# Optimization experiments

Hardware: AMD Instinct MI355X
Metric: run time of the kernel (lower is better)

## Reference

```python
import jax, jax.numpy as jnp
import numpy as np

TEMP1, TEMP2, TEMP3 = 4.0, 5.0, 10.0  # forward() default temps
EPS = 1e-8


def setup_inputs() -> dict:
    key = jax.random.key(0)
    k1, k2 = jax.random.split(key)
    B, L, D = 64, 64, 512
    return {
        "ecg_embs": jax.random.normal(k1, (B, L, D), dtype=jnp.float32),
        "sent_embs": jax.random.normal(k2, (B, L, D), dtype=jnp.float32),
    }


def reference(ecg_embs, sent_embs):
    # Fully-batched version of the original per-sample Python loop.
    # i indexes the sentence (query) sample, j the ecg (context) sample.
    B, L, D = ecg_embs.shape
    # scores[i,j,s,q] = <ecg[j,s,:], sent[i,q,:]>  == contextT @ query in torch
    scores = jnp.einsum('jsd,iqd->ijsq', ecg_embs, sent_embs)
    # 1st softmax over query axis q
    attn = jax.nn.softmax(scores, axis=-1)
    # transpose to (i,j,q,s), temperature-scale, 2nd softmax over source axis s
    attn = jax.nn.softmax(TEMP1 * jnp.swapaxes(attn, -1, -2), axis=-1)  # (i,j,q,s)
    # weightedContext[i,j,q,:] = sum_s attn[i,j,q,s] * ecg[j,s,:]
    wctx = jnp.einsum('ijqs,jsd->ijqd', attn, ecg_embs)
    sent = sent_embs[:, None]  # (i,1,q,d) broadcast over j
    w12 = jnp.sum(sent * wctx, axis=-1)
    w1 = jnp.linalg.norm(sent, axis=-1)
    w2 = jnp.linalg.norm(wctx, axis=-1)
    cos = w12 / jnp.maximum(w1 * w2, EPS)  # (i,j,q)
    # row_sim.mul_(temp2).exp_().sum(dim=1).log() ; similarities[j,i] (cat along dim=1)
    sim = TEMP3 * jnp.log(jnp.sum(jnp.exp(TEMP2 * cos), axis=-1)).T  # (j,i)
    labels = jnp.arange(B)
    logp0 = jax.nn.log_softmax(sim, axis=-1)
    logp1 = jax.nn.log_softmax(sim.T, axis=-1)
    loss0 = -jnp.mean(logp0[labels, labels])
    loss1 = -jnp.mean(logp1[labels, labels])
    # att_maps: list of attn[i] from iteration i == diagonal (i==j) attention,
    # each shaped (1, queryL, ih=1, iw=sourceL); stacked -> (B, 1, L, 1, L)
    att_maps = attn[labels, labels][:, None, :, None, :]
    return (loss0 + loss1) / 2.0, att_maps
```

## Files before the change

### kernel.cpp

```cpp
#include <hip/hip_runtime.h>
#include <math.h>

typedef __attribute__((ext_vector_type(8))) short short8;
typedef __attribute__((ext_vector_type(4))) float f32x4;
typedef unsigned int uint;
typedef unsigned short ushort;

#define T1 4.0f
#define T2 5.0f
#define T3 10.0f
#define EPSF 1e-8f
#define SST 68

__device__ inline ushort f2bf(float x) {
    union { float f; uint u; } a; a.f = x;
    uint r = a.u + 0x7FFFu + ((a.u >> 16) & 1u);
    return (ushort)(r >> 16);
}
__device__ inline float bf2f(ushort h) {
    union { uint u; float f; } a; a.u = ((uint)h) << 16;
    return a.f;
}

#define GLDS(gsrc, ldst) \
    __builtin_amdgcn_global_load_lds( \
        (const __attribute__((address_space(1))) uint*)(gsrc), \
        (__attribute__((address_space(3))) uint*)(ldst), 16, 0, 0)

__global__ __launch_bounds__(256) void prep_kernel(
        const float* __restrict__ ecg, const float* __restrict__ sent,
        char* __restrict__ EH, char* __restrict__ EL,
        char* __restrict__ SH, char* __restrict__ SL, float* __restrict__ w1) {
    __shared__ float partial[256];
    const int bid = blockIdx.x;
    const int tensor = bid >> 6, idx = bid & 63;
    const float* src = (tensor ? sent : ecg) + (size_t)idx * 32768;
    char* dh = (tensor ? SH : EH) + (size_t)idx * 65536;
    char* dl = (tensor ? SL : EL) + (size_t)idx * 65536;
    const int tid = threadIdx.x;
    const int r = tid & 63;
    float s2 = 0.f;
    #pragma unroll
    for (int it = 0; it < 4; it++) {
        int kc = it * 4 + (tid >> 6);
        const float* p = src + r * 512 + kc * 32;
        char* oh = dh + kc * 4096 + r * 64;
        char* ol = dl + kc * 4096 + r * 64;
        #pragma unroll
        for (int c = 0; c < 4; c++) {
            float4 v0 = *(const float4*)(p + c * 8);
            float4 v1 = *(const float4*)(p + c * 8 + 4);
            float x[8] = {v0.x, v0.y, v0.z, v0.w, v1.x, v1.y, v1.z, v1.w};
            uint hw[4], lw[4];
            #pragma unroll
            for (int e = 0; e < 4; e++) {
                float a0 = x[2 * e], a1 = x[2 * e + 1];
                ushort h0 = f2bf(a0), h1 = f2bf(a1);
                hw[e] = (uint)h0 | ((uint)h1 << 16);
                ushort l0 = f2bf(a0 - bf2f(h0)), l1 = f2bf(a1 - bf2f(h1));
                lw[e] = (uint)l0 | ((uint)l1 << 16);
                s2 += a0 * a0 + a1 * a1;
            }
            int phys = (c + (r >> 1)) & 3;
            uint4 H; H.x = hw[0]; H.y = hw[1]; H.z = hw[2]; H.w = hw[3];
            *(uint4*)(oh + phys * 16) = H;
            uint4 L; L.x = lw[0]; L.y = lw[1]; L.z = lw[2]; L.w = lw[3];
            *(uint4*)(ol + phys * 16) = L;
        }
    }
    partial[tid] = s2;
    __syncthreads();
    if (tensor == 1 && tid < 64) {
        float t = partial[tid] + partial[tid + 64] + partial[tid + 128] + partial[tid + 192];
        w1[idx * 64 + tid] = sqrtf(t);
    }
}

__global__ __launch_bounds__(256) void gprep_kernel(
        const char* __restrict__ EH, const char* __restrict__ EL, char* __restrict__ Gp) {
    __shared__ __align__(16) char lds[8192];
    const int j = blockIdx.x;
    const int tid = threadIdx.x;
    const int wv = tid >> 6, lane = tid & 63;
    const int wq = wv >> 1, wn = wv & 1;
    const int quad = lane >> 4, ln = lane & 15;
    const char* srcH = EH + (size_t)j * 65536 + wv * 1024 + lane * 16;
    const char* srcL = EL + (size_t)j * 65536 + wv * 1024 + lane * 16;

    int ao[2], bo[2];
    #pragma unroll
    for (int mi = 0; mi < 2; mi++) {
        int R = 32 * wq + 16 * mi + ln;
        ao[mi] = R * 64 + ((quad + (R >> 1)) & 3) * 16;
    }
    #pragma unroll
    for (int ni = 0; ni < 2; ni++) {
        int R = 32 * wn + 16 * ni + ln;
        bo[ni] = R * 64 + ((quad + (R >> 1)) & 3) * 16;
    }

    f32x4 acc[2][2];
    #pragma unroll
    for (int a = 0; a < 2; a++)
        #pragma unroll
        for (int b = 0; b < 2; b++) acc[a][b] = (f32x4){0.f, 0.f, 0.f, 0.f};

    for (int kc = 0; kc < 16; kc++) {
        GLDS(srcH + (size_t)kc * 4096, lds + wv * 1024);
        GLDS(srcL + (size_t)kc * 4096, lds + 4096 + wv * 1024);
        __syncthreads();
        short8 ah[2], al[2], bh[2], bl[2];
        #pragma unroll
        for (int mi = 0; mi < 2; mi++) {
            ah[mi] = *(const short8*)(lds + ao[mi]);
            al[mi] = *(const short8*)(lds + 4096 + ao[mi]);
        }
        #pragma unroll
        for (int ni = 0; ni < 2; ni++) {
            bh[ni] = *(const short8*)(lds + bo[ni]);
            bl[ni] = *(const short8*)(lds + 4096 + bo[ni]);
        }
        #pragma unroll
        for (int mi = 0; mi < 2; mi++)
            #pragma unroll
            for (int ni = 0; ni < 2; ni++) {
                acc[mi][ni] = __builtin_amdgcn_mfma_f32_16x16x32_bf16(ah[mi], bh[ni], acc[mi][ni], 0, 0, 0);
                acc[mi][ni] = __builtin_amdgcn_mfma_f32_16x16x32_bf16(ah[mi], bl[ni], acc[mi][ni], 0, 0, 0);
                acc[mi][ni] = __builtin_amdgcn_mfma_f32_16x16x32_bf16(al[mi], bh[ni], acc[mi][ni], 0, 0, 0);
            }
        __syncthreads();
    }
    #pragma unroll
    for (int mi = 0; mi < 2; mi++)
        #pragma unroll
        for (int ni = 0; ni < 2; ni++)
            #pragma unroll
            for (int r = 0; r < 4; r++) {
                int t = 32 * wq + 16 * mi + quad * 4 + r;
                int u = 32 * wn + 16 * ni + ln;
                float g = acc[mi][ni][r];
                ushort h = f2bf(g);
                ushort l = f2bf(g - bf2f(h));
                char* base = Gp + (size_t)j * 16384 + t * 128 + (((u >> 3) + t) & 7) * 16 + (u & 7) * 2;
                *(ushort*)base = h;
                *(ushort*)(base + 8192) = l;
            }
}

__global__ __launch_bounds__(256, 4) void pair_kernel(
        const char* __restrict__ EH, const char* __restrict__ EL,
        const char* __restrict__ SH, const char* __restrict__ SL,
        const char* __restrict__ Gp, const float* __restrict__ w1g,
        float* __restrict__ simval, float* __restrict__ out) {

    __shared__ __align__(16) char lds[33792];
    __shared__ __align__(16) float mz[64];
    __shared__ float w12all[256], w2all[256];

    const int tid = threadIdx.x;
    const int bn = blockIdx.x;
    const int xcd = bn & 7, slot = bn >> 3;
    const int T = xcd * 8 + (slot >> 4);
    const int wp = slot & 15;
    const int bi = (T >> 3) * 4 + (wp >> 2);
    const int bj = (T & 7) * 4 + (wp & 3);
    const int i0 = bi * 2, j0 = bj * 2;

    const int wv = tid >> 6, lane = tid & 63;
    const int wq = wv >> 1, wn = wv & 1;
    const int quad = lane >> 4, ln = lane & 15;

    int aoff[4], boff[4];
    #pragma unroll
    for (int mi = 0; mi < 4; mi++) {
        int R = 64 * (mi >> 1) + 32 * wq + 16 * (mi & 1) + ln;
        aoff[mi] = R * 64 + ((quad + (R >> 1)) & 3) * 16;
    }
    #pragma unroll
    for (int ni = 0; ni < 4; ni++) {
        int R = 64 * (ni >> 1) + 32 * wn + 16 * (ni & 1) + ln;
        boff[ni] = 16384 + R * 64 + ((quad + (R >> 1)) & 3) * 16;
    }

    const char* gA; const char* gB; int ldoff;
    if (wv == 0)      { gA = EH + (size_t)j0 * 65536;       gB = EH + (size_t)(j0 + 1) * 65536; ldoff = 0; }
    else if (wv == 1) { gA = EL + (size_t)j0 * 65536;       gB = EL + (size_t)(j0 + 1) * 65536; ldoff = 8192; }
    else if (wv == 2) { gA = SH + (size_t)i0 * 65536;       gB = SH + (size_t)(i0 + 1) * 65536; ldoff = 16384; }
    else              { gA = SL + (size_t)i0 * 65536;       gB = SL + (size_t)(i0 + 1) * 65536; ldoff = 24576; }
    gA += lane * 16; gB += lane * 16;

    f32x4 acc[4][4];
    #pragma unroll
    for (int a = 0; a < 4; a++)
        #pragma unroll
        for (int b = 0; b < 4; b++) acc[a][b] = (f32x4){0.f, 0.f, 0.f, 0.f};

    for (int kc = 0; kc < 16; kc++) {
        #pragma unroll
        for (int n = 0; n < 4; n++) GLDS(gA + n * 1024, lds + ldoff + n * 1024);
        #pragma unroll
        for (int n = 0; n < 4; n++) GLDS(gB + n * 1024, lds + ldoff + 4096 + n * 1024);
        gA += 4096; gB += 4096;
        __syncthreads();
        short8 bh[4], bl[4];
        #pragma unroll
        for (int ni = 0; ni < 4; ni++) {
            bh[ni] = *(const short8*)(lds + boff[ni]);
            bl[ni] = *(const short8*)(lds + boff[ni] + 8192);
        }
        #pragma unroll
        for (int mi = 0; mi < 4; mi++) {
            short8 ah = *(const short8*)(lds + aoff[mi]);
            short8 al = *(const short8*)(lds + aoff[mi] + 8192);
            #pragma unroll
            for (int ni = 0; ni < 4; ni++) {
                acc[mi][ni] = __builtin_amdgcn_mfma_f32_16x16x32_bf16(ah, bh[ni], acc[mi][ni], 0, 0, 0);
                acc[mi][ni] = __builtin_amdgcn_mfma_f32_16x16x32_bf16(ah, bl[ni], acc[mi][ni], 0, 0, 0);
                acc[mi][ni] = __builtin_amdgcn_mfma_f32_16x16x32_bf16(al, bh[ni], acc[mi][ni], 0, 0, 0);
            }
        }
        __syncthreads();
    }

    float* SsT = (float*)lds;
    float* yT  = (float*)lds;
    char*  Pb  = lds + 17408;

    #pragma unroll
    for (int pr = 0; pr < 4; pr++) {
        const int a = pr >> 1, b = pr & 1;
        const int i = i0 + b, j = j0 + a;

        #pragma unroll
        for (int dm = 0; dm < 2; dm++)
            #pragma unroll
            for (int dn = 0; dn < 2; dn++) {
                int s0 = 32 * wq + 16 * dm + quad * 4;
                int q  = 32 * wn + 16 * dn + ln;
                *(f32x4*)(SsT + q * SST + s0) = acc[2 * a + dm][2 * b + dn];
            }
        __syncthreads();

        {
            const int s = tid >> 2, c = tid & 3;
            float vv[16]; float m = -1e30f;
            #pragma unroll
            for (int t = 0; t < 16; t++) { vv[t] = SsT[(16 * c + t) * SST + s]; m = fmaxf(m, vv[t]); }
            m = fmaxf(m, __shfl_xor(m, 1));
            m = fmaxf(m, __shfl_xor(m, 2));
            float sum = 0.f;
            #pragma unroll
            for (int t = 0; t < 16; t++) sum += __expf(vv[t] - m);
            sum += __shfl_xor(sum, 1);
            sum += __shfl_xor(sum, 2);
            if (c == 0) mz[s] = m + __logf(sum);
        }
        __syncthreads();

        {
            const int q = tid >> 2, c = tid & 3;
            float sc[16], at[16];
            #pragma unroll
            for (int r4 = 0; r4 < 4; r4++)
                *(f32x4*)(sc + 4 * r4) = *(const f32x4*)(SsT + q * SST + 16 * c + 4 * r4);
            float mzv[16];
            #pragma unroll
            for (int r4 = 0; r4 < 4; r4++)
                *(f32x4*)(mzv + 4 * r4) = *(const f32x4*)(mz + 16 * c + 4 * r4);
            float m2 = -1e30f;
            #pragma unroll
            for (int t = 0; t < 16; t++) {
                at[t] = __expf(sc[t] - mzv[t]);
                m2 = fmaxf(m2, T1 * at[t]);
            }
            m2 = fmaxf(m2, __shfl_xor(m2, 1));
            m2 = fmaxf(m2, __shfl_xor(m2, 2));
            float sum = 0.f;
            #pragma unroll
            for (int t = 0; t < 16; t++) { at[t] = __expf(T1 * at[t] - m2); sum += at[t]; }
            sum += __shfl_xor(sum, 1);
            sum += __shfl_xor(sum, 2);
            float inv = 1.f / sum;
            float p12 = 0.f;
            #pragma unroll
            for (int t = 0; t < 16; t++) { at[t] *= inv; p12 += at[t] * sc[t]; }
            p12 += __shfl_xor(p12, 1);
            p12 += __shfl_xor(p12, 2);
            if (c == 0) w12all[pr * 64 + q] = p12;

            if (i == j) {
                float* om = out + 1 + (size_t)i * 4096;
                #pragma unroll
                for (int t = 0; t < 16; t++) om[q * 64 + c * 16 + t] = at[t];
            }

            uint hw[8], lw[8];
            #pragma unroll
            for (int e = 0; e < 8; e++) {
                ushort h0 = f2bf(at[2 * e]), h1 = f2bf(at[2 * e + 1]);
                hw[e] = (uint)h0 | ((uint)h1 << 16);
                ushort l0 = f2bf(at[2 * e] - bf2f(h0)), l1 = f2bf(at[2 * e + 1] - bf2f(h1));
                lw[e] = (uint)l0 | ((uint)l1 << 16);
            }
            int p0 = (2 * c + q) & 7, p1 = (2 * c + 1 + q) & 7;
            uint4 W;
            W.x = hw[0]; W.y = hw[1]; W.z = hw[2]; W.w = hw[3];
            *(uint4*)(Pb + q * 128 + p0 * 16) = W;
            W.x = hw[4]; W.y = hw[5]; W.z = hw[6]; W.w = hw[7];
            *(uint4*)(Pb + q * 128 + p1 * 16) = W;
            W.x = lw[0]; W.y = lw[1]; W.z = lw[2]; W.w = lw[3];
            *(uint4*)(Pb + 8192 + q * 128 + p0 * 16) = W;
            W.x = lw[4]; W.y = lw[5]; W.z = lw[6]; W.w = lw[7];
            *(uint4*)(Pb + 8192 + q * 128 + p1 * 16) = W;
        }
        __syncthreads();

        {
            const char* gs = Gp + (size_t)j * 16384 + tid * 64;
            char* gd = lds + tid * 64;
            uint4 g0 = *(const uint4*)(gs);
            uint4 g1 = *(const uint4*)(gs + 16);
            uint4 g2 = *(const uint4*)(gs + 32);
            uint4 g3 = *(const uint4*)(gs + 48);
            *(uint4*)(gd)      = g0;
            *(uint4*)(gd + 16) = g1;
            *(uint4*)(gd + 32) = g2;
            *(uint4*)(gd + 48) = g3;
        }
        __syncthreads();

        f32x4 acc2[2][2];
        #pragma unroll
        for (int x = 0; x < 2; x++)
            #pragma unroll
            for (int y = 0; y < 2; y++) acc2[x][y] = (f32x4){0.f, 0.f, 0.f, 0.f};
        #pragma unroll
        for (int ch = 0; ch < 2; ch++) {
            short8 pah[2], pal[2], gbh[2], gbl[2];
            #pragma unroll
            for (int m2i = 0; m2i < 2; m2i++) {
                int q = 32 * wq + 16 * m2i + ln;
                int ph = ((ch * 4 + quad) + q) & 7;
                pah[m2i] = *(const short8*)(Pb + q * 128 + ph * 16);
                pal[m2i] = *(const short8*)(Pb + 8192 + q * 128 + ph * 16);
            }
            #pragma unroll
            for (int n2i = 0; n2i < 2; n2i++) {
                int u = 32 * wn + 16 * n2i + ln;
                int ph = ((ch * 4 + quad) + u) & 7;
                gbh[n2i] = *(const short8*)(lds + u * 128 + ph * 16);
                gbl[n2i] = *(const short8*)(lds + 8192 + u * 128 + ph * 16);
            }
            #pragma unroll
            for (int m2i = 0; m2i < 2; m2i++)
                #pragma unroll
                for (int n2i = 0; n2i < 2; n2i++) {
                    acc2[m2i][n2i] = __builtin_amdgcn_mfma_f32_16x16x32_bf16(pah[m2i], gbh[n2i], acc2[m2i][n2i], 0, 0, 0);
                    acc2[m2i][n2i] = __builtin_amdgcn_mfma_f32_16x16x32_bf16(pah[m2i], gbl[n2i], acc2[m2i][n2i], 0, 0, 0);
                    acc2[m2i][n2i] = __builtin_amdgcn_mfma_f32_16x16x32_bf16(pal[m2i], gbh[n2i], acc2[m2i][n2i], 0, 0, 0);
                }
        }
        __syncthreads();

        #pragma unroll
        for (int m2i = 0; m2i < 2; m2i++)
            #pragma unroll
            for (int n2i = 0; n2i < 2; n2i++) {
                int q0 = 32 * wq + 16 * m2i + quad * 4;
                int t  = 32 * wn + 16 * n2i + ln;
                *(f32x4*)(yT + t * SST + q0) = acc2[m2i][n2i];
            }
        __syncthreads();

        {
            const int q = tid >> 2, c = tid & 3;
            int p0 = (2 * c + q) & 7, p1 = (2 * c + 1 + q) & 7;
            uint4 H0 = *(const uint4*)(Pb + q * 128 + p0 * 16);
            uint4 H1 = *(const uint4*)(Pb + q * 128 + p1 * 16);
            uint4 L0 = *(const uint4*)(Pb + 8192 + q * 128 + p0 * 16);
            uint4 L1 = *(const uint4*)(Pb + 8192 + q * 128 + p1 * 16);
            uint hw[8] = {H0.x,H0.y,H0.z,H0.w, H1.x,H1.y,H1.z,H1.w};
            uint lw[8] = {L0.x,L0.y,L0.z,L0.w, L1.x,L1.y,L1.z,L1.w};
            float s = 0.f;
            #pragma unroll
            for (int e = 0; e < 8; e++) {
                float q0v = bf2f((ushort)(hw[e] & 0xFFFFu)) + bf2f((ushort)(lw[e] & 0xFFFFu));
                float q1v = bf2f((ushort)(hw[e] >> 16))     + bf2f((ushort)(lw[e] >> 16));
                s += q0v * yT[(16 * c + 2 * e) * SST + q];
                s += q1v * yT[(16 * c + 2 * e + 1) * SST + q];
            }
            s += __shfl_xor(s, 1);
            s += __shfl_xor(s, 2);
            if (c == 0) w2all[pr * 64 + q] = s;
        }
        __syncthreads();
    }

    {
        const int pr = wv;
        const int ii = i0 + (pr & 1), jj = j0 + (pr >> 1);
        float w2 = sqrtf(fmaxf(w2all[pr * 64 + lane], 0.f));
        float cosv = w12all[pr * 64 + lane] / fmaxf(w1g[ii * 64 + lane] * w2, EPSF);
        float e = __expf(T2 * cosv);
        #pragma unroll
        for (int off = 32; off; off >>= 1) e += __shfl_down(e, off);
        if (lane == 0) simval[ii * 64 + jj] = T3 * __logf(e);
    }
}

__global__ __launch_bounds__(256) void loss_kernel(const float* __restrict__ val,
                                                   float* __restrict__ out) {
    __shared__ float v[4096];
    const int tid = threadIdx.x;
    #pragma unroll
    for (int k = 0; k < 4; k++)
        ((float4*)v)[tid + k * 256] = ((const float4*)val)[tid + k * 256];
    __syncthreads();
    if (tid < 64) {
        int i = tid;
        float rmax = -1e30f, cmax = -1e30f;
        for (int jj = 0; jj < 64; jj++) {
            rmax = fmaxf(rmax, v[i * 64 + jj]);
            cmax = fmaxf(cmax, v[jj * 64 + i]);
        }
        float rs = 0.f, cs = 0.f;
        for (int jj = 0; jj < 64; jj++) {
            rs += __expf(v[i * 64 + jj] - rmax);
            cs += __expf(v[jj * 64 + i] - cmax);
        }
        float rlse = rmax + __logf(rs);
        float clse = cmax + __logf(cs);
        float part = 2.f * v[i * 64 + i] - rlse - clse;
        #pragma unroll
        for (int off = 32; off; off >>= 1) part += __shfl_down(part, off);
        if (i == 0) out[0] = -part / 128.f;
    }
}

extern "C" void kernel_launch(void* const* d_in, const int* in_sizes, int n_in,
                              void* d_out, int out_size, void* d_ws, size_t ws_size,
                              hipStream_t stream) {
    (void)in_sizes; (void)n_in; (void)out_size; (void)ws_size;
    const float* ecg  = (const float*)d_in[0];
    const float* sent = (const float*)d_in[1];
    float* out = (float*)d_out;

    char* ws = (char*)d_ws;
    float* w1v  = (float*)ws;
    float* simv = (float*)(ws + 16384);
    char* EH = ws + 32768;
    char* EL = EH + (size_t)64 * 65536;
    char* SH = EL + (size_t)64 * 65536;
    char* SL = SH + (size_t)64 * 65536;
    char* Gp = SL + (size_t)64 * 65536;

    prep_kernel <<<128, 256, 0, stream>>>(ecg, sent, EH, EL, SH, SL, w1v);
    gprep_kernel<<<64,  256, 0, stream>>>(EH, EL, Gp);
    pair_kernel <<<1024, 256, 0, stream>>>(EH, EL, SH, SL, Gp, w1v, simv, out);
    loss_kernel <<<1,   256, 0, stream>>>(simv, out);
}
```

Before: 151.3 us.

## Fuse prep and Gram kernels, drop attention low-part split, read Gram from global

Merges the bf16 hi/lo split prep kernel with the Gram-matrix kernel, so ecg blocks compute G directly from freshly converted tiles and one launch plus a global round trip disappear. In the pair kernel the attention matrix is now stored only as a bf16 high part, which cuts one of three MFMAs in the second GEMM. Gram operands are read straight from global/L2 instead of being staged through LDS. The w2 quadratic form is computed from the accumulators in registers with a small partial-sum buffer, and the score tile uses an XOR-swizzled layout, removing several barriers and LDS passes. Dropping the attention low part lowers precision of w2, and direct global loads of G may add latency.

```diff
diff --git a/kernel.cpp b/kernel.cpp
--- a/kernel.cpp
+++ b/kernel.cpp
@@ -10,7 +10,6 @@
 #define T2 5.0f
 #define T3 10.0f
 #define EPSF 1e-8f
-#define SST 68
 
 __device__ inline ushort f2bf(float x) {
     union { float f; uint u; } a; a.f = x;
@@ -27,124 +26,127 @@
         (const __attribute__((address_space(1))) uint*)(gsrc), \
         (__attribute__((address_space(3))) uint*)(ldst), 16, 0, 0)
 
-__global__ __launch_bounds__(256) void prep_kernel(
+__global__ __launch_bounds__(256) void prepg_kernel(
         const float* __restrict__ ecg, const float* __restrict__ sent,
         char* __restrict__ EH, char* __restrict__ EL,
-        char* __restrict__ SH, char* __restrict__ SL, float* __restrict__ w1) {
-    __shared__ float partial[256];
+        char* __restrict__ SH, char* __restrict__ SL,
+        char* __restrict__ Gp, float* __restrict__ w1) {
+    __shared__ __align__(16) char plds[8192];
     const int bid = blockIdx.x;
-    const int tensor = bid >> 6, idx = bid & 63;
-    const float* src = (tensor ? sent : ecg) + (size_t)idx * 32768;
-    char* dh = (tensor ? SH : EH) + (size_t)idx * 65536;
-    char* dl = (tensor ? SL : EL) + (size_t)idx * 65536;
     const int tid = threadIdx.x;
-    const int r = tid & 63;
-    float s2 = 0.f;
-    #pragma unroll
-    for (int it = 0; it < 4; it++) {
-        int kc = it * 4 + (tid >> 6);
-        const float* p = src + r * 512 + kc * 32;
-        char* oh = dh + kc * 4096 + r * 64;
-        char* ol = dl + kc * 4096 + r * 64;
-        #pragma unroll
-        for (int c = 0; c < 4; c++) {
-            float4 v0 = *(const float4*)(p + c * 8);
-            float4 v1 = *(const float4*)(p + c * 8 + 4);
-            float x[8] = {v0.x, v0.y, v0.z, v0.w, v1.x, v1.y, v1.z, v1.w};
-            uint hw[4], lw[4];
-            #pragma unroll
-            for (int e = 0; e < 4; e++) {
-                float a0 = x[2 * e], a1 = x[2 * e + 1];
-                ushort h0 = f2bf(a0), h1 = f2bf(a1);
-                hw[e] = (uint)h0 | ((uint)h1 << 16);
-                ushort l0 = f2bf(a0 - bf2f(h0)), l1 = f2bf(a1 - bf2f(h1));
-                lw[e] = (uint)l0 | ((uint)l1 << 16);
-                s2 += a0 * a0 + a1 * a1;
-            }
-            int phys = (c + (r >> 1)) & 3;
-            uint4 H; H.x = hw[0]; H.y = hw[1]; H.z = hw[2]; H.w = hw[3];
-            *(uint4*)(oh + phys * 16) = H;
-            uint4 L; L.x = lw[0]; L.y = lw[1]; L.z = lw[2]; L.w = lw[3];
-            *(uint4*)(ol + phys * 16) = L;
-        }
-    }
-    partial[tid] = s2;
-    __syncthreads();
-    if (tensor == 1 && tid < 64) {
-        float t = partial[tid] + partial[tid + 64] + partial[tid + 128] + partial[tid + 192];
-        w1[idx * 64 + tid] = sqrtf(t);
-    }
-}
-
-__global__ __launch_bounds__(256) void gprep_kernel(
-        const char* __restrict__ EH, const char* __restrict__ EL, char* __restrict__ Gp) {
-    __shared__ __align__(16) char lds[8192];
-    const int j = blockIdx.x;
-    const int tid = threadIdx.x;
-    const int wv = tid >> 6, lane = tid & 63;
-    const int wq = wv >> 1, wn = wv & 1;
-    const int quad = lane >> 4, ln = lane & 15;
-    const char* srcH = EH + (size_t)j * 65536 + wv * 1024 + lane * 16;
-    const char* srcL = EL + (size_t)j * 65536 + wv * 1024 + lane * 16;
-
-    int ao[2], bo[2];
-    #pragma unroll
-    for (int mi = 0; mi < 2; mi++) {
-        int R = 32 * wq + 16 * mi + ln;
-        ao[mi] = R * 64 + ((quad + (R >> 1)) & 3) * 16;
-    }
-    #pragma unroll
-    for (int ni = 0; ni < 2; ni++) {
-        int R = 32 * wn + 16 * ni + ln;
-        bo[ni] = R * 64 + ((quad + (R >> 1)) & 3) * 16;
-    }
-
-    f32x4 acc[2][2];
-    #pragma unroll
-    for (int a = 0; a < 2; a++)
-        #pragma unroll
-        for (int b = 0; b < 2; b++) acc[a][b] = (f32x4){0.f, 0.f, 0.f, 0.f};
-
-    for (int kc = 0; kc < 16; kc++) {
-        GLDS(srcH + (size_t)kc * 4096, lds + wv * 1024);
-        GLDS(srcL + (size_t)kc * 4096, lds + 4096 + wv * 1024);
-        __syncthreads();
-        short8 ah[2], al[2], bh[2], bl[2];
+    const int r = tid >> 2, cq = tid & 3;
+    const int phys = (cq + (r >> 1)) & 3;
+
+    if (bid < 64) {
+        const int j = bid;
+        const float* src = ecg + (size_t)j * 32768;
+        char* dh = EH + (size_t)j * 65536;
+        char* dl = EL + (size_t)j * 65536;
+        const int wv = tid >> 6, lane = tid & 63;
+        const int wq = wv >> 1, wn = wv & 1;
+        const int quad = lane >> 4, ln = lane & 15;
+        int ao[2], bo[2];
         #pragma unroll
         for (int mi = 0; mi < 2; mi++) {
-            ah[mi] = *(const short8*)(lds + ao[mi]);
-            al[mi] = *(const short8*)(lds + 4096 + ao[mi]);
+            int R = 32 * wq + 16 * mi + ln;
+            ao[mi] = R * 64 + ((quad + (R >> 1)) & 3) * 16;
         }
         #pragma unroll
         for (int ni = 0; ni < 2; ni++) {
-            bh[ni] = *(const short8*)(lds + bo[ni]);
-            bl[ni] = *(const short8*)(lds + 4096 + bo[ni]);
+            int R = 32 * wn + 16 * ni + ln;
+            bo[ni] = R * 64 + ((quad + (R >> 1)) & 3) * 16;
+        }
+        f32x4 acc[2][2];
+        #pragma unroll
+        for (int a = 0; a < 2; a++)
+            #pragma unroll
+            for (int b = 0; b < 2; b++) acc[a][b] = (f32x4){0.f, 0.f, 0.f, 0.f};
+
+        for (int kc = 0; kc < 16; kc++) {
+            const float4* p = (const float4*)(src + (size_t)r * 512 + kc * 32 + cq * 8);
+            float4 va = p[0], vb = p[1];
+            ushort h0 = f2bf(va.x), h1 = f2bf(va.y), h2 = f2bf(va.z), h3 = f2bf(va.w);
+            ushort h4 = f2bf(vb.x), h5 = f2bf(vb.y), h6 = f2bf(vb.z), h7 = f2bf(vb.w);
+            uint4 H;
+            H.x = (uint)h0 | ((uint)h1 << 16); H.y = (uint)h2 | ((uint)h3 << 16);
+            H.z = (uint)h4 | ((uint)h5 << 16); H.w = (uint)h6 | ((uint)h7 << 16);
+            uint4 L;
+            L.x = (uint)f2bf(va.x - bf2f(h0)) | ((uint)f2bf(va.y - bf2f(h1)) << 16);
+            L.y = (uint)f2bf(va.z - bf2f(h2)) | ((uint)f2bf(va.w - bf2f(h3)) << 16);
+            L.z = (uint)f2bf(vb.x - bf2f(h4)) | ((uint)f2bf(vb.y - bf2f(h5)) << 16);
+            L.w = (uint)f2bf(vb.z - bf2f(h6)) | ((uint)f2bf(vb.w - bf2f(h7)) << 16);
+            __syncthreads();
+            *(uint4*)(plds + r * 64 + phys * 16)        = H;
+            *(uint4*)(plds + 4096 + r * 64 + phys * 16) = L;
+            *(uint4*)(dh + (size_t)kc * 4096 + r * 64 + phys * 16) = H;
+            *(uint4*)(dl + (size_t)kc * 4096 + r * 64 + phys * 16) = L;
+            __syncthreads();
+            short8 ah[2], al[2], bh[2], bl[2];
+            #pragma unroll
+            for (int mi = 0; mi < 2; mi++) {
+                ah[mi] = *(const short8*)(plds + ao[mi]);
+                al[mi] = *(const short8*)(plds + 4096 + ao[mi]);
+            }
+            #pragma unroll
+            for (int ni = 0; ni < 2; ni++) {
+                bh[ni] = *(const short8*)(plds + bo[ni]);
+                bl[ni] = *(const short8*)(plds + 4096 + bo[ni]);
+            }
+            #pragma unroll
+            for (int mi = 0; mi < 2; mi++)
+                #pragma unroll
+                for (int ni = 0; ni < 2; ni++) {
+                    acc[mi][ni] = __builtin_amdgcn_mfma_f32_16x16x32_bf16(ah[mi], bh[ni], acc[mi][ni], 0, 0, 0);
+                    acc[mi][ni] = __builtin_amdgcn_mfma_f32_16x16x32_bf16(ah[mi], bl[ni], acc[mi][ni], 0, 0, 0);
+                    acc[mi][ni] = __builtin_amdgcn_mfma_f32_16x16x32_bf16(al[mi], bh[ni], acc[mi][ni], 0, 0, 0);
+                }
         }
         #pragma unroll
         for (int mi = 0; mi < 2; mi++)
             #pragma unroll
-            for (int ni = 0; ni < 2; ni++) {
-                acc[mi][ni] = __builtin_amdgcn_mfma_f32_16x16x32_bf16(ah[mi], bh[ni], acc[mi][ni], 0, 0, 0);
-                acc[mi][ni] = __builtin_amdgcn_mfma_f32_16x16x32_bf16(ah[mi], bl[ni], acc[mi][ni], 0, 0, 0);
-                acc[mi][ni] = __builtin_amdgcn_mfma_f32_16x16x32_bf16(al[mi], bh[ni], acc[mi][ni], 0, 0, 0);
-            }
-        __syncthreads();
-    }
-    #pragma unroll
-    for (int mi = 0; mi < 2; mi++)
-        #pragma unroll
-        for (int ni = 0; ni < 2; ni++)
-            #pragma unroll
-            for (int r = 0; r < 4; r++) {
-                int t = 32 * wq + 16 * mi + quad * 4 + r;
-                int u = 32 * wn + 16 * ni + ln;
-                float g = acc[mi][ni][r];
-                ushort h = f2bf(g);
-                ushort l = f2bf(g - bf2f(h));
-                char* base = Gp + (size_t)j * 16384 + t * 128 + (((u >> 3) + t) & 7) * 16 + (u & 7) * 2;
-                *(ushort*)base = h;
-                *(ushort*)(base + 8192) = l;
-            }
+            for (int ni = 0; ni < 2; ni++)
+                #pragma unroll
+                for (int rr = 0; rr < 4; rr++) {
+                    int t = 32 * wq + 16 * mi + quad * 4 + rr;
+                    int u = 32 * wn + 16 * ni + ln;
+                    float g = acc[mi][ni][rr];
+                    ushort h = f2bf(g);
+                    ushort l = f2bf(g - bf2f(h));
+                    char* base = Gp + (size_t)j * 16384 + t * 128 + (((u >> 3) + t) & 7) * 16 + (u & 7) * 2;
+                    *(ushort*)base = h;
+                    *(ushort*)(base + 8192) = l;
+                }
+    } else {
+        const int idx = bid - 64;
+        const float* src = sent + (size_t)idx * 32768;
+        char* dh = SH + (size_t)idx * 65536;
+        char* dl = SL + (size_t)idx * 65536;
+        float s2 = 0.f;
+        for (int kc = 0; kc < 16; kc++) {
+            const float4* p = (const float4*)(src + (size_t)r * 512 + kc * 32 + cq * 8);
+            float4 va = p[0], vb = p[1];
+            s2 += va.x * va.x + va.y * va.y + va.z * va.z + va.w * va.w +
+                  vb.x * vb.x + vb.y * vb.y + vb.z * vb.z + vb.w * vb.w;
+            ushort h0 = f2bf(va.x), h1 = f2bf(va.y), h2 = f2bf(va.z), h3 = f2bf(va.w);
+            ushort h4 = f2bf(vb.x), h5 = f2bf(vb.y), h6 = f2bf(vb.z), h7 = f2bf(vb.w);
+            uint4 H;
+            H.x = (uint)h0 | ((uint)h1 << 16); H.y = (uint)h2 | ((uint)h3 << 16);
+            H.z = (uint)h4 | ((uint)h5 << 16); H.w = (uint)h6 | ((uint)h7 << 16);
+            uint4 L;
+            L.x = (uint)f2bf(va.x - bf2f(h0)) | ((uint)f2bf(va.y - bf2f(h1)) << 16);
+            L.y = (uint)f2bf(va.z - bf2f(h2)) | ((uint)f2bf(va.w - bf2f(h3)) << 16);
+            L.z = (uint)f2bf(vb.x - bf2f(h4)) | ((uint)f2bf(vb.y - bf2f(h5)) << 16);
+            L.w = (uint)f2bf(vb.z - bf2f(h6)) | ((uint)f2bf(vb.w - bf2f(h7)) << 16);
+            *(uint4*)(dh + (size_t)kc * 4096 + r * 64 + phys * 16) = H;
+            *(uint4*)(dl + (size_t)kc * 4096 + r * 64 + phys * 16) = L;
+        }
+        ((float*)plds)[tid] = s2;
+        __syncthreads();
+        if (tid < 64) {
+            const float* q = (const float*)plds + tid * 4;
+            w1[idx * 64 + tid] = sqrtf(q[0] + q[1] + q[2] + q[3]);
+        }
+    }
 }
 
 __global__ __launch_bounds__(256, 4) void pair_kernel(
@@ -153,9 +155,10 @@
         const char* __restrict__ Gp, const float* __restrict__ w1g,
         float* __restrict__ simval, float* __restrict__ out) {
 
-    __shared__ __align__(16) char lds[33792];
+    __shared__ __align__(16) char lds[32768];
     __shared__ __align__(16) float mz[64];
     __shared__ float w12all[256], w2all[256];
+    __shared__ float w2part[64 * 9];
 
     const int tid = threadIdx.x;
     const int bn = blockIdx.x;
@@ -222,14 +225,13 @@
         __syncthreads();
     }
 
-    float* SsT = (float*)lds;
-    float* yT  = (float*)lds;
-    char*  Pb  = lds + 17408;
+    char* Phi = lds + 16384;
 
     #pragma unroll
     for (int pr = 0; pr < 4; pr++) {
         const int a = pr >> 1, b = pr & 1;
         const int i = i0 + b, j = j0 + a;
+        const char* Gpj = Gp + (size_t)j * 16384;
 
         #pragma unroll
         for (int dm = 0; dm < 2; dm++)
@@ -237,7 +239,7 @@
             for (int dn = 0; dn < 2; dn++) {
                 int s0 = 32 * wq + 16 * dm + quad * 4;
                 int q  = 32 * wn + 16 * dn + ln;
-                *(f32x4*)(SsT + q * SST + s0) = acc[2 * a + dm][2 * b + dn];
+                *(f32x4*)(lds + q * 256 + (((s0 >> 2) + q) & 15) * 16) = acc[2 * a + dm][2 * b + dn];
             }
         __syncthreads();
 
@@ -245,7 +247,11 @@
             const int s = tid >> 2, c = tid & 3;
             float vv[16]; float m = -1e30f;
             #pragma unroll
-            for (int t = 0; t < 16; t++) { vv[t] = SsT[(16 * c + t) * SST + s]; m = fmaxf(m, vv[t]); }
+            for (int t = 0; t < 16; t++) {
+                int q = 16 * c + t;
+                vv[t] = *(const float*)(lds + q * 256 + ((((s >> 2) + q) & 15) << 4) + ((s & 3) << 2));
+                m = fmaxf(m, vv[t]);
+            }
             m = fmaxf(m, __shfl_xor(m, 1));
             m = fmaxf(m, __shfl_xor(m, 2));
             float sum = 0.f;
@@ -259,14 +265,13 @@
 
         {
             const int q = tid >> 2, c = tid & 3;
-            float sc[16], at[16];
-            #pragma unroll
-            for (int r4 = 0; r4 < 4; r4++)
-                *(f32x4*)(sc + 4 * r4) = *(const f32x4*)(SsT + q * SST + 16 * c + 4 * r4);
-            float mzv[16];
-            #pragma unroll
-            for (int r4 = 0; r4 < 4; r4++)
-                *(f32x4*)(mzv + 4 * r4) = *(const f32x4*)(mz + 16 * c + 4 * r4);
+            float sc[16], at[16], mzv[16];
+            #pragma unroll
+            for (int k = 0; k < 4; k++)
+                *(f32x4*)(sc + 4 * k) = *(const f32x4*)(lds + q * 256 + (((4 * c + k) + q) & 15) * 16);
+            #pragma unroll
+            for (int k = 0; k < 4; k++)
+                *(f32x4*)(mzv + 4 * k) = *(const f32x4*)(mz + 16 * c + 4 * k);
             float m2 = -1e30f;
             #pragma unroll
             for (int t = 0; t < 16; t++) {
@@ -294,38 +299,16 @@
                 for (int t = 0; t < 16; t++) om[q * 64 + c * 16 + t] = at[t];
             }
 
-            uint hw[8], lw[8];
-            #pragma unroll
-            for (int e = 0; e < 8; e++) {
-                ushort h0 = f2bf(at[2 * e]), h1 = f2bf(at[2 * e + 1]);
-                hw[e] = (uint)h0 | ((uint)h1 << 16);
-                ushort l0 = f2bf(at[2 * e] - bf2f(h0)), l1 = f2bf(at[2 * e + 1] - bf2f(h1));
-                lw[e] = (uint)l0 | ((uint)l1 << 16);
-            }
+            uint hw[8];
+            #pragma unroll
+            for (int e = 0; e < 8; e++)
+                hw[e] = (uint)f2bf(at[2 * e]) | ((uint)f2bf(at[2 * e + 1]) << 16);
             int p0 = (2 * c + q) & 7, p1 = (2 * c + 1 + q) & 7;
             uint4 W;
             W.x = hw[0]; W.y = hw[1]; W.z = hw[2]; W.w = hw[3];
-            *(uint4*)(Pb + q * 128 + p0 * 16) = W;
+            *(uint4*)(Phi + q * 128 + p0 * 16) = W;
             W.x = hw[4]; W.y = hw[5]; W.z = hw[6]; W.w = hw[7];
-            *(uint4*)(Pb + q * 128 + p1 * 16) = W;
-            W.x = lw[0]; W.y = lw[1]; W.z = lw[2]; W.w = lw[3];
-            *(uint4*)(Pb + 8192 + q * 128 + p0 * 16) = W;
-            W.x = lw[4]; W.y = lw[5]; W.z = lw[6]; W.w = lw[7];
-            *(uint4*)(Pb + 8192 + q * 128 + p1 * 16) = W;
-        }
-        __syncthreads();
-
-        {
-            const char* gs = Gp + (size_t)j * 16384 + tid * 64;
-            char* gd = lds + tid * 64;
-            uint4 g0 = *(const uint4*)(gs);
-            uint4 g1 = *(const uint4*)(gs + 16);
-            uint4 g2 = *(const uint4*)(gs + 32);
-            uint4 g3 = *(const uint4*)(gs + 48);
-            *(uint4*)(gd)      = g0;
-            *(uint4*)(gd + 16) = g1;
-            *(uint4*)(gd + 32) = g2;
-            *(uint4*)(gd + 48) = g3;
+            *(uint4*)(Phi + q * 128 + p1 * 16) = W;
         }
         __syncthreads();
 
@@ -336,20 +319,18 @@
             for (int y = 0; y < 2; y++) acc2[x][y] = (f32x4){0.f, 0.f, 0.f, 0.f};
         #pragma unroll
         for (int ch = 0; ch < 2; ch++) {
-            short8 pah[2], pal[2], gbh[2], gbl[2];
+            short8 pah[2], gbh[2], gbl[2];
             #pragma unroll
             for (int m2i = 0; m2i < 2; m2i++) {
                 int q = 32 * wq + 16 * m2i + ln;
-                int ph = ((ch * 4 + quad) + q) & 7;
-                pah[m2i] = *(const short8*)(Pb + q * 128 + ph * 16);
-                pal[m2i] = *(const short8*)(Pb + 8192 + q * 128 + ph * 16);
+                pah[m2i] = *(const short8*)(Phi + q * 128 + (((ch * 4 + quad) + q) & 7) * 16);
             }
             #pragma unroll
             for (int n2i = 0; n2i < 2; n2i++) {
                 int u = 32 * wn + 16 * n2i + ln;
                 int ph = ((ch * 4 + quad) + u) & 7;
-                gbh[n2i] = *(const short8*)(lds + u * 128 + ph * 16);
-                gbl[n2i] = *(const short8*)(lds + 8192 + u * 128 + ph * 16);
+                gbh[n2i] = *(const short8*)(Gpj + u * 128 + ph * 16);
+                gbl[n2i] = *(const short8*)(Gpj + 8192 + u * 128 + ph * 16);
             }
             #pragma unroll
             for (int m2i = 0; m2i < 2; m2i++)
@@ -357,44 +338,35 @@
                 for (int n2i = 0; n2i < 2; n2i++) {
                     acc2[m2i][n2i] = __builtin_amdgcn_mfma_f32_16x16x32_bf16(pah[m2i], gbh[n2i], acc2[m2i][n2i], 0, 0, 0);
                     acc2[m2i][n2i] = __builtin_amdgcn_mfma_f32_16x16x32_bf16(pah[m2i], gbl[n2i], acc2[m2i][n2i], 0, 0, 0);
-                    acc2[m2i][n2i] = __builtin_amdgcn_mfma_f32_16x16x32_bf16(pal[m2i], gbh[n2i], acc2[m2i][n2i], 0, 0, 0);
                 }
         }
-        __syncthreads();
 
         #pragma unroll
         for (int m2i = 0; m2i < 2; m2i++)
             #pragma unroll
-            for (int n2i = 0; n2i < 2; n2i++) {
-                int q0 = 32 * wq + 16 * m2i + quad * 4;
-                int t  = 32 * wn + 16 * n2i + ln;
-                *(f32x4*)(yT + t * SST + q0) = acc2[m2i][n2i];
-            }
-        __syncthreads();
-
-        {
-            const int q = tid >> 2, c = tid & 3;
-            int p0 = (2 * c + q) & 7, p1 = (2 * c + 1 + q) & 7;
-            uint4 H0 = *(const uint4*)(Pb + q * 128 + p0 * 16);
-            uint4 H1 = *(const uint4*)(Pb + q * 128 + p1 * 16);
-            uint4 L0 = *(const uint4*)(Pb + 8192 + q * 128 + p0 * 16);
-            uint4 L1 = *(const uint4*)(Pb + 8192 + q * 128 + p1 * 16);
-            uint hw[8] = {H0.x,H0.y,H0.z,H0.w, H1.x,H1.y,H1.z,H1.w};
-            uint lw[8] = {L0.x,L0.y,L0.z,L0.w, L1.x,L1.y,L1.z,L1.w};
-            float s = 0.f;
-            #pragma unroll
-            for (int e = 0; e < 8; e++) {
-                float q0v = bf2f((ushort)(hw[e] & 0xFFFFu)) + bf2f((ushort)(lw[e] & 0xFFFFu));
-                float q1v = bf2f((ushort)(hw[e] >> 16))     + bf2f((ushort)(lw[e] >> 16));
-                s += q0v * yT[(16 * c + 2 * e) * SST + q];
-                s += q1v * yT[(16 * c + 2 * e + 1) * SST + q];
-            }
-            s += __shfl_xor(s, 1);
-            s += __shfl_xor(s, 2);
-            if (c == 0) w2all[pr * 64 + q] = s;
-        }
-        __syncthreads();
-    }
+            for (int rr = 0; rr < 4; rr++) {
+                int q = 32 * wq + 16 * m2i + quad * 4 + rr;
+                float p = 0.f;
+                #pragma unroll
+                for (int n2i = 0; n2i < 2; n2i++) {
+                    int t = 32 * wn + 16 * n2i + ln;
+                    float Pv = bf2f(*(const ushort*)(Phi + q * 128 +
+                                     ((((t >> 3) + q) & 7) << 4) + ((t & 7) << 1)));
+                    p += acc2[m2i][n2i][rr] * Pv;
+                }
+                p += __shfl_xor(p, 1);
+                p += __shfl_xor(p, 2);
+                if ((ln & 3) == 0) w2part[q * 9 + wn * 4 + (ln >> 2)] = p;
+            }
+        __syncthreads();
+
+        if (tid < 64) {
+            const float* wp9 = w2part + tid * 9;
+            w2all[pr * 64 + tid] = wp9[0] + wp9[1] + wp9[2] + wp9[3] +
+                                   wp9[4] + wp9[5] + wp9[6] + wp9[7];
+        }
+    }
+    __syncthreads();
 
     {
         const int pr = wv;
@@ -454,8 +426,7 @@
     char* SL = SH + (size_t)64 * 65536;
     char* Gp = SL + (size_t)64 * 65536;
 
-    prep_kernel <<<128, 256, 0, stream>>>(ecg, sent, EH, EL, SH, SL, w1v);
-    gprep_kernel<<<64,  256, 0, stream>>>(EH, EL, Gp);
+    prepg_kernel<<<128,  256, 0, stream>>>(ecg, sent, EH, EL, SH, SL, Gp, w1v);
     pair_kernel <<<1024, 256, 0, stream>>>(EH, EL, SH, SL, Gp, w1v, simv, out);
-    loss_kernel <<<1,   256, 0, stream>>>(simv, out);
-}
+    loss_kernel <<<1,    256, 0, stream>>>(simv, out);
+}
```

Result: slower. 158.7 us (+4.9%).
